# Optimization experiments

Measured on AMD Instinct MI355X. Metric: run time of the kernel, lower is better.

The kernel has to match this reference:

```python
import jax, jax.numpy as jnp
import numpy as np

B, I, H = 64, 1024, 1024
WSCALE = 0.02  # approx Xavier std for 1024-dim fan-in/out


def setup_inputs() -> dict:
    key = jax.random.key(0)
    ks = jax.random.split(key, 9)
    return {
        "input": jax.random.normal(ks[0], (B, I), jnp.float32),
        "h": jax.random.normal(ks[1], (B, H), jnp.float32),
        "C": jax.random.normal(ks[2], (B, H, H), jnp.float32),
        "weight_ih": jax.random.normal(ks[3], (3 * H, I), jnp.float32) * WSCALE,
        "weight_hh": jax.random.normal(ks[4], (3 * H, H), jnp.float32) * WSCALE,
        "bias": jnp.zeros((3 * H,), jnp.float32),
        "Wq_w": jax.random.normal(ks[5], (H, I), jnp.float32) * WSCALE,
        "Wq_b": jnp.zeros((H,), jnp.float32),
        "Wk_w": jax.random.normal(ks[6], (H, I), jnp.float32) * WSCALE,
        "Wk_b": jnp.zeros((H,), jnp.float32),
        "Wv_w": jax.random.normal(ks[7], (H, I), jnp.float32) * WSCALE,
        "Wv_b": jnp.zeros((H,), jnp.float32),
    }


def reference(input, h, C, weight_ih, weight_hh, bias, Wq_w, Wq_b, Wk_w, Wk_b, Wv_w, Wv_b):
    # gates: [B, 3H]
    gates = input @ weight_ih.T + bias + h @ weight_hh.T
    i, f, o = jnp.split(gates, 3, axis=1)
    i = jnp.exp(i)
    f = jnp.exp(f)
    o = jax.nn.sigmoid(o)
    q = input @ Wq_w.T + Wq_b
    k = input @ Wk_w.T + Wk_b
    v = input @ Wv_w.T + Wv_b
    # matrix memory update: outer product v k^T gated by i, decay by f (broadcast over columns)
    C_new = f[:, :, None] * C + i[:, :, None] * (v[:, :, None] * k[:, None, :])
    # readout: h = o * (q^T C_new), contracting q over the row (v) axis of C
    h_new = o * jnp.einsum("bi,bij->bj", q, C_new)
    return (h_new, C_new)
```

## Files before the change

### kernel.cpp

```cpp
#include <hip/hip_runtime.h>
#include <math.h>

typedef float v4 __attribute__((ext_vector_type(4)));
typedef float f32x4 __attribute__((ext_vector_type(4)));
typedef __bf16 bf16x8 __attribute__((ext_vector_type(8)));

#define HD 1024
#define NB 64

#define WS_IGT  0
#define WS_FGT  65536
#define WS_QT   131072
#define WS_VT   196608
#define WS_OGN  262144
#define WS_KN   327680
#define WS_BPK  393216
#define WS_PART 458752

__global__ __launch_bounds__(256) void k_prepb(const float* __restrict__ input,
                                               const float* __restrict__ h,
                                               float* __restrict__ ws) {
    int o = blockIdx.x * 256 + threadIdx.x;
    int l  = o & 63;
    int bt = (o >> 6) & 3;
    int ks = o >> 8;
    const float* srcm = (ks < 32) ? input : h;
    const float* src = srcm + (size_t)(bt * 16 + (l & 15)) * HD + (ks & 31) * 32 + (l >> 4) * 8;
    v4 f0 = *(const v4*)src;
    v4 f1 = *(const v4*)(src + 4);
    bf16x8 pk;
    pk[0] = (__bf16)f0.x; pk[1] = (__bf16)f0.y; pk[2] = (__bf16)f0.z; pk[3] = (__bf16)f0.w;
    pk[4] = (__bf16)f1.x; pk[5] = (__bf16)f1.y; pk[6] = (__bf16)f1.z; pk[7] = (__bf16)f1.w;
    *((bf16x8*)((__bf16*)(ws + WS_BPK)) + o) = pk;
}

__global__ __launch_bounds__(256) void k_gemm(
    const float* __restrict__ Wih, const float* __restrict__ Whh, const float* __restrict__ bias,
    const float* __restrict__ Wq, const float* __restrict__ Wqb,
    const float* __restrict__ Wk, const float* __restrict__ Wkb,
    const float* __restrict__ Wv, const float* __restrict__ Wvb,
    float* __restrict__ ws) {
    int tid  = threadIdx.x;
    int lane = tid & 63;
    int w    = tid >> 6;
    int t    = blockIdx.x;

    const bf16x8* Bp = (const bf16x8*)((const __bf16*)(ws + WS_BPK));
    __shared__ f32x4 red[4][4][64];

    f32x4 a0 = {0.f, 0.f, 0.f, 0.f};
    f32x4 a1 = a0, a2 = a0, a3 = a0;

    if (t < 192) {
        int row = t * 16 + (lane & 15);
        const float* Wb = (w < 2) ? Wih : Whh;
        const float* wrow = Wb + (size_t)row * HD + (lane >> 4) * 8;
        int cofs = (w < 2) ? 0 : -1024;
        int s0 = w * 16;
        #pragma unroll 4
        for (int s = 0; s < 16; ++s) {
            int ks = s0 + s;
            const float* ap = wrow + ks * 32 + cofs;
            v4 f0 = *(const v4*)ap;
            v4 f1 = *(const v4*)(ap + 4);
            bf16x8 a;
            a[0] = (__bf16)f0.x; a[1] = (__bf16)f0.y; a[2] = (__bf16)f0.z; a[3] = (__bf16)f0.w;
            a[4] = (__bf16)f1.x; a[5] = (__bf16)f1.y; a[6] = (__bf16)f1.z; a[7] = (__bf16)f1.w;
            const bf16x8* bb = Bp + (size_t)ks * 256 + lane;
            bf16x8 b0 = bb[0], b1 = bb[64], b2 = bb[128], b3 = bb[192];
            a0 = __builtin_amdgcn_mfma_f32_16x16x32_bf16(a, b0, a0, 0, 0, 0);
            a1 = __builtin_amdgcn_mfma_f32_16x16x32_bf16(a, b1, a1, 0, 0, 0);
            a2 = __builtin_amdgcn_mfma_f32_16x16x32_bf16(a, b2, a2, 0, 0, 0);
            a3 = __builtin_amdgcn_mfma_f32_16x16x32_bf16(a, b3, a3, 0, 0, 0);
        }
    } else {
        int t2  = t - 192;
        int sel = t2 >> 6;
        const float* W = (sel == 0) ? Wq : (sel == 1) ? Wk : Wv;
        int row = (t2 & 63) * 16 + (lane & 15);
        const float* wrow = W + (size_t)row * HD + (lane >> 4) * 8;
        int s0 = w * 8;
        #pragma unroll 4
        for (int s = 0; s < 8; ++s) {
            int ks = s0 + s;
            const float* ap = wrow + ks * 32;
            v4 f0 = *(const v4*)ap;
            v4 f1 = *(const v4*)(ap + 4);
            bf16x8 a;
            a[0] = (__bf16)f0.x; a[1] = (__bf16)f0.y; a[2] = (__bf16)f0.z; a[3] = (__bf16)f0.w;
            a[4] = (__bf16)f1.x; a[5] = (__bf16)f1.y; a[6] = (__bf16)f1.z; a[7] = (__bf16)f1.w;
            const bf16x8* bb = Bp + (size_t)ks * 256 + lane;
            bf16x8 b0 = bb[0], b1 = bb[64], b2 = bb[128], b3 = bb[192];
            a0 = __builtin_amdgcn_mfma_f32_16x16x32_bf16(a, b0, a0, 0, 0, 0);
            a1 = __builtin_amdgcn_mfma_f32_16x16x32_bf16(a, b1, a1, 0, 0, 0);
            a2 = __builtin_amdgcn_mfma_f32_16x16x32_bf16(a, b2, a2, 0, 0, 0);
            a3 = __builtin_amdgcn_mfma_f32_16x16x32_bf16(a, b3, a3, 0, 0, 0);
        }
    }

    red[w][0][lane] = a0;
    red[w][1][lane] = a1;
    red[w][2][lane] = a2;
    red[w][3][lane] = a3;
    __syncthreads();

    int b    = tid & 63;
    int rgrp = tid >> 6;
    int lane2 = (rgrp << 4) | (b & 15);
    int bt    = b >> 4;
    f32x4 s4 = red[0][bt][lane2];
    s4 += red[1][bt][lane2];
    s4 += red[2][bt][lane2];
    s4 += red[3][bt][lane2];

    if (t < 192) {
        int seg  = t >> 6;
        int rloc = (t & 63) * 16 + rgrp * 4;
        int rg   = t * 16 + rgrp * 4;
        if (seg == 0) {
            #pragma unroll
            for (int q = 0; q < 4; ++q)
                ws[WS_IGT + (rloc + q) * 64 + b] = expf(s4[q] + bias[rg + q]);
        } else if (seg == 1) {
            #pragma unroll
            for (int q = 0; q < 4; ++q)
                ws[WS_FGT + (rloc + q) * 64 + b] = expf(s4[q] + bias[rg + q]);
        } else {
            v4 o;
            #pragma unroll
            for (int q = 0; q < 4; ++q) {
                float x = s4[q] + bias[rg + q];
                o[q] = 1.f / (1.f + expf(-x));
            }
            *(v4*)(ws + WS_OGN + b * HD + rloc) = o;
        }
    } else {
        int t2   = t - 192;
        int sel  = t2 >> 6;
        int rloc = (t2 & 63) * 16 + rgrp * 4;
        const float* Bv = (sel == 0) ? Wqb : (sel == 1) ? Wkb : Wvb;
        if (sel == 0) {
            #pragma unroll
            for (int q = 0; q < 4; ++q)
                ws[WS_QT + (rloc + q) * 64 + b] = s4[q] + Bv[rloc + q];
        } else if (sel == 1) {
            v4 kv;
            #pragma unroll
            for (int q = 0; q < 4; ++q) kv[q] = s4[q] + Bv[rloc + q];
            *(v4*)(ws + WS_KN + b * HD + rloc) = kv;
        } else {
            #pragma unroll
            for (int q = 0; q < 4; ++q)
                ws[WS_VT + (rloc + q) * 64 + b] = s4[q] + Bv[rloc + q];
        }
    }
}

__global__ __launch_bounds__(256) void k_update(const float* __restrict__ C,
                                                float* __restrict__ out,
                                                float* __restrict__ ws) {
    int b  = blockIdx.x >> 5;
    int c  = blockIdx.x & 31;
    int i0 = c << 5;
    int tid = threadIdx.x;

    __shared__ float fg_s[32], iv_s[32], q_s[32];
    if (tid < 32) {
        int i = i0 + tid;
        fg_s[tid] = ws[WS_FGT + i * 64 + b];
        iv_s[tid] = ws[WS_IGT + i * 64 + b] * ws[WS_VT + i * 64 + b];
        q_s[tid]  = ws[WS_QT + i * 64 + b];
    }
    __syncthreads();

    v4 k4 = *(const v4*)(ws + WS_KN + b * HD + tid * 4);
    const v4* Cb = (const v4*)(C + (size_t)b * HD * HD) + tid;
    v4*       On = (v4*)(out + NB * HD + (size_t)b * HD * HD) + tid;
    v4 acc0 = {0.f, 0.f, 0.f, 0.f};
    v4 acc1 = {0.f, 0.f, 0.f, 0.f};

    #pragma unroll
    for (int ii = 0; ii < 32; ii += 4) {
        size_t r0 = (size_t)(i0 + ii) * 256;
        v4 c0 = __builtin_nontemporal_load(&Cb[r0]);
        v4 c1 = __builtin_nontemporal_load(&Cb[r0 + 256]);
        v4 c2 = __builtin_nontemporal_load(&Cb[r0 + 512]);
        v4 c3 = __builtin_nontemporal_load(&Cb[r0 + 768]);

        float f0 = fg_s[ii + 0], g0 = iv_s[ii + 0], q0 = q_s[ii + 0];
        float f1 = fg_s[ii + 1], g1 = iv_s[ii + 1], q1 = q_s[ii + 1];
        float f2 = fg_s[ii + 2], g2 = iv_s[ii + 2], q2 = q_s[ii + 2];
        float f3 = fg_s[ii + 3], g3 = iv_s[ii + 3], q3 = q_s[ii + 3];

        v4 n0, n1, n2, n3;
        n0.x = f0 * c0.x + g0 * k4.x; n0.y = f0 * c0.y + g0 * k4.y;
        n0.z = f0 * c0.z + g0 * k4.z; n0.w = f0 * c0.w + g0 * k4.w;
        n1.x = f1 * c1.x + g1 * k4.x; n1.y = f1 * c1.y + g1 * k4.y;
        n1.z = f1 * c1.z + g1 * k4.z; n1.w = f1 * c1.w + g1 * k4.w;
        n2.x = f2 * c2.x + g2 * k4.x; n2.y = f2 * c2.y + g2 * k4.y;
        n2.z = f2 * c2.z + g2 * k4.z; n2.w = f2 * c2.w + g2 * k4.w;
        n3.x = f3 * c3.x + g3 * k4.x; n3.y = f3 * c3.y + g3 * k4.y;
        n3.z = f3 * c3.z + g3 * k4.z; n3.w = f3 * c3.w + g3 * k4.w;

        __builtin_nontemporal_store(n0, &On[r0]);
        __builtin_nontemporal_store(n1, &On[r0 + 256]);
        __builtin_nontemporal_store(n2, &On[r0 + 512]);
        __builtin_nontemporal_store(n3, &On[r0 + 768]);

        acc0.x += q0 * n0.x; acc0.y += q0 * n0.y; acc0.z += q0 * n0.z; acc0.w += q0 * n0.w;
        acc1.x += q1 * n1.x; acc1.y += q1 * n1.y; acc1.z += q1 * n1.z; acc1.w += q1 * n1.w;
        acc0.x += q2 * n2.x; acc0.y += q2 * n2.y; acc0.z += q2 * n2.z; acc0.w += q2 * n2.w;
        acc1.x += q3 * n3.x; acc1.y += q3 * n3.y; acc1.z += q3 * n3.z; acc1.w += q3 * n3.w;
    }
    v4 acc;
    acc.x = acc0.x + acc1.x; acc.y = acc0.y + acc1.y;
    acc.z = acc0.z + acc1.z; acc.w = acc0.w + acc1.w;
    *(v4*)(ws + WS_PART + (size_t)(c * 64 + b) * HD + tid * 4) = acc;
}

__global__ __launch_bounds__(256) void k_final(float* __restrict__ out,
                                               const float* __restrict__ ws) {
    int b = blockIdx.x;
    int tid = threadIdx.x;
    const v4* part = (const v4*)(ws + WS_PART);
    v4 s = {0.f, 0.f, 0.f, 0.f};
    #pragma unroll 4
    for (int c = 0; c < 32; ++c) {
        v4 p = part[(size_t)(c * 64 + b) * 256 + tid];
        s.x += p.x; s.y += p.y; s.z += p.z; s.w += p.w;
    }
    v4 o4 = *(const v4*)(ws + WS_OGN + b * HD + tid * 4);
    v4 r;
    r.x = o4.x * s.x; r.y = o4.y * s.y; r.z = o4.z * s.z; r.w = o4.w * s.w;
    *(v4*)(out + b * HD + tid * 4) = r;
}

extern "C" void kernel_launch(void* const* d_in, const int* in_sizes, int n_in,
                              void* d_out, int out_size, void* d_ws, size_t ws_size,
                              hipStream_t stream) {
    const float* input = (const float*)d_in[0];
    const float* h     = (const float*)d_in[1];
    const float* C     = (const float*)d_in[2];
    const float* Wih   = (const float*)d_in[3];
    const float* Whh   = (const float*)d_in[4];
    const float* bias  = (const float*)d_in[5];
    const float* Wq_w  = (const float*)d_in[6];
    const float* Wq_b  = (const float*)d_in[7];
    const float* Wk_w  = (const float*)d_in[8];
    const float* Wk_b  = (const float*)d_in[9];
    const float* Wv_w  = (const float*)d_in[10];
    const float* Wv_b  = (const float*)d_in[11];
    float* out = (float*)d_out;
    float* ws  = (float*)d_ws;

    k_prepb<<<64, 256, 0, stream>>>(input, h, ws);
    k_gemm<<<384, 256, 0, stream>>>(Wih, Whh, bias, Wq_w, Wq_b, Wk_w, Wk_b, Wv_w, Wv_b, ws);
    k_update<<<2048, 256, 0, stream>>>(C, out, ws);
    k_final<<<64, 256, 0, stream>>>(out, ws);
}
```

Baseline: 480.8 us.

## Split projection GEMM into split-K waves with separate activation reduction kernel

```diff
diff --git a/kernel.cpp b/kernel.cpp
--- a/kernel.cpp
+++ b/kernel.cpp
@@ -16,6 +16,8 @@
 #define WS_KN   327680
 #define WS_BPK  393216
 #define WS_PART 458752
+#define WS_PG   2555904
+#define WS_PQ   5701632
 
 __global__ __launch_bounds__(256) void k_prepb(const float* __restrict__ input,
                                                const float* __restrict__ h,
@@ -34,125 +36,88 @@
     *((bf16x8*)((__bf16*)(ws + WS_BPK)) + o) = pk;
 }
 
-__global__ __launch_bounds__(256) void k_gemm(
-    const float* __restrict__ Wih, const float* __restrict__ Whh, const float* __restrict__ bias,
-    const float* __restrict__ Wq, const float* __restrict__ Wqb,
-    const float* __restrict__ Wk, const float* __restrict__ Wkb,
-    const float* __restrict__ Wv, const float* __restrict__ Wvb,
+__global__ __launch_bounds__(256) void k_mfma(
+    const float* __restrict__ Wih, const float* __restrict__ Whh,
+    const float* __restrict__ Wq, const float* __restrict__ Wk, const float* __restrict__ Wv,
     float* __restrict__ ws) {
-    int tid  = threadIdx.x;
-    int lane = tid & 63;
-    int w    = tid >> 6;
-    int t    = blockIdx.x;
-
+    int lane = threadIdx.x & 63;
+    int w = blockIdx.x * 4 + (threadIdx.x >> 6);
     const bf16x8* Bp = (const bf16x8*)((const __bf16*)(ws + WS_BPK));
-    __shared__ f32x4 red[4][4][64];
+
+    const float* wrow;
+    float* pout;
+    int ksB;
+    if (w < 3072) {
+        int t = w >> 4, c = w & 15;
+        const float* Wb = (c < 8) ? Wih : Whh;
+        int kk0 = (c & 7) * 128;
+        wrow = Wb + (size_t)(t * 16 + (lane & 15)) * HD + kk0 + (lane >> 4) * 8;
+        pout = ws + WS_PG + (size_t)(c * 192 + t) * 1024;
+        ksB  = c * 4;
+    } else {
+        int w2 = w - 3072;
+        int t = w2 >> 3, c = w2 & 7;
+        int sel = t >> 6;
+        const float* W = (sel == 0) ? Wq : (sel == 1) ? Wk : Wv;
+        wrow = W + (size_t)((t & 63) * 16 + (lane & 15)) * HD + c * 128 + (lane >> 4) * 8;
+        pout = ws + WS_PQ + (size_t)(c * 192 + t) * 1024;
+        ksB  = c * 4;
+    }
 
     f32x4 a0 = {0.f, 0.f, 0.f, 0.f};
     f32x4 a1 = a0, a2 = a0, a3 = a0;
-
-    if (t < 192) {
-        int row = t * 16 + (lane & 15);
-        const float* Wb = (w < 2) ? Wih : Whh;
-        const float* wrow = Wb + (size_t)row * HD + (lane >> 4) * 8;
-        int cofs = (w < 2) ? 0 : -1024;
-        int s0 = w * 16;
-        #pragma unroll 4
-        for (int s = 0; s < 16; ++s) {
-            int ks = s0 + s;
-            const float* ap = wrow + ks * 32 + cofs;
-            v4 f0 = *(const v4*)ap;
-            v4 f1 = *(const v4*)(ap + 4);
-            bf16x8 a;
-            a[0] = (__bf16)f0.x; a[1] = (__bf16)f0.y; a[2] = (__bf16)f0.z; a[3] = (__bf16)f0.w;
-            a[4] = (__bf16)f1.x; a[5] = (__bf16)f1.y; a[6] = (__bf16)f1.z; a[7] = (__bf16)f1.w;
-            const bf16x8* bb = Bp + (size_t)ks * 256 + lane;
-            bf16x8 b0 = bb[0], b1 = bb[64], b2 = bb[128], b3 = bb[192];
-            a0 = __builtin_amdgcn_mfma_f32_16x16x32_bf16(a, b0, a0, 0, 0, 0);
-            a1 = __builtin_amdgcn_mfma_f32_16x16x32_bf16(a, b1, a1, 0, 0, 0);
-            a2 = __builtin_amdgcn_mfma_f32_16x16x32_bf16(a, b2, a2, 0, 0, 0);
-            a3 = __builtin_amdgcn_mfma_f32_16x16x32_bf16(a, b3, a3, 0, 0, 0);
-        }
+    #pragma unroll
+    for (int s = 0; s < 4; ++s) {
+        const float* ap = wrow + s * 32;
+        v4 f0 = *(const v4*)ap;
+        v4 f1 = *(const v4*)(ap + 4);
+        bf16x8 a;
+        a[0] = (__bf16)f0.x; a[1] = (__bf16)f0.y; a[2] = (__bf16)f0.z; a[3] = (__bf16)f0.w;
+        a[4] = (__bf16)f1.x; a[5] = (__bf16)f1.y; a[6] = (__bf16)f1.z; a[7] = (__bf16)f1.w;
+        const bf16x8* bb = Bp + (size_t)(ksB + s) * 256 + lane;
+        bf16x8 b0 = bb[0], b1 = bb[64], b2 = bb[128], b3 = bb[192];
+        a0 = __builtin_amdgcn_mfma_f32_16x16x32_bf16(a, b0, a0, 0, 0, 0);
+        a1 = __builtin_amdgcn_mfma_f32_16x16x32_bf16(a, b1, a1, 0, 0, 0);
+        a2 = __builtin_amdgcn_mfma_f32_16x16x32_bf16(a, b2, a2, 0, 0, 0);
+        a3 = __builtin_amdgcn_mfma_f32_16x16x32_bf16(a, b3, a3, 0, 0, 0);
+    }
+    int rb = (lane >> 4) * 4, cb = lane & 15;
+    #pragma unroll
+    for (int q = 0; q < 4; ++q) {
+        pout[(rb + q) * 64 +  0 + cb] = a0[q];
+        pout[(rb + q) * 64 + 16 + cb] = a1[q];
+        pout[(rb + q) * 64 + 32 + cb] = a2[q];
+        pout[(rb + q) * 64 + 48 + cb] = a3[q];
+    }
+}
+
+__global__ __launch_bounds__(256) void k_act(
+    const float* __restrict__ bias,
+    const float* __restrict__ Wqb, const float* __restrict__ Wkb, const float* __restrict__ Wvb,
+    float* __restrict__ ws) {
+    int g = blockIdx.x * 256 + threadIdx.x;
+    if (g < 196608) {
+        int r = g >> 6, b = g & 63;
+        int t = r >> 4, ro = r & 15;
+        const float* P = ws + WS_PG + ro * 64 + b;
+        float s = bias[r];
+        #pragma unroll
+        for (int c = 0; c < 16; ++c) s += P[(size_t)(c * 192 + t) * 1024];
+        if (r < 1024)       ws[WS_IGT + r * 64 + b] = expf(s);
+        else if (r < 2048)  ws[WS_FGT + (r - 1024) * 64 + b] = expf(s);
+        else                ws[WS_OGN + b * HD + (r - 2048)] = 1.f / (1.f + expf(-s));
     } else {
-        int t2  = t - 192;
-        int sel = t2 >> 6;
-        const float* W = (sel == 0) ? Wq : (sel == 1) ? Wk : Wv;
-        int row = (t2 & 63) * 16 + (lane & 15);
-        const float* wrow = W + (size_t)row * HD + (lane >> 4) * 8;
-        int s0 = w * 8;
-        #pragma unroll 4
-        for (int s = 0; s < 8; ++s) {
-            int ks = s0 + s;
-            const float* ap = wrow + ks * 32;
-            v4 f0 = *(const v4*)ap;
-            v4 f1 = *(const v4*)(ap + 4);
-            bf16x8 a;
-            a[0] = (__bf16)f0.x; a[1] = (__bf16)f0.y; a[2] = (__bf16)f0.z; a[3] = (__bf16)f0.w;
-            a[4] = (__bf16)f1.x; a[5] = (__bf16)f1.y; a[6] = (__bf16)f1.z; a[7] = (__bf16)f1.w;
-            const bf16x8* bb = Bp + (size_t)ks * 256 + lane;
-            bf16x8 b0 = bb[0], b1 = bb[64], b2 = bb[128], b3 = bb[192];
-            a0 = __builtin_amdgcn_mfma_f32_16x16x32_bf16(a, b0, a0, 0, 0, 0);
-            a1 = __builtin_amdgcn_mfma_f32_16x16x32_bf16(a, b1, a1, 0, 0, 0);
-            a2 = __builtin_amdgcn_mfma_f32_16x16x32_bf16(a, b2, a2, 0, 0, 0);
-            a3 = __builtin_amdgcn_mfma_f32_16x16x32_bf16(a, b3, a3, 0, 0, 0);
-        }
-    }
-
-    red[w][0][lane] = a0;
-    red[w][1][lane] = a1;
-    red[w][2][lane] = a2;
-    red[w][3][lane] = a3;
-    __syncthreads();
-
-    int b    = tid & 63;
-    int rgrp = tid >> 6;
-    int lane2 = (rgrp << 4) | (b & 15);
-    int bt    = b >> 4;
-    f32x4 s4 = red[0][bt][lane2];
-    s4 += red[1][bt][lane2];
-    s4 += red[2][bt][lane2];
-    s4 += red[3][bt][lane2];
-
-    if (t < 192) {
-        int seg  = t >> 6;
-        int rloc = (t & 63) * 16 + rgrp * 4;
-        int rg   = t * 16 + rgrp * 4;
-        if (seg == 0) {
-            #pragma unroll
-            for (int q = 0; q < 4; ++q)
-                ws[WS_IGT + (rloc + q) * 64 + b] = expf(s4[q] + bias[rg + q]);
-        } else if (seg == 1) {
-            #pragma unroll
-            for (int q = 0; q < 4; ++q)
-                ws[WS_FGT + (rloc + q) * 64 + b] = expf(s4[q] + bias[rg + q]);
-        } else {
-            v4 o;
-            #pragma unroll
-            for (int q = 0; q < 4; ++q) {
-                float x = s4[q] + bias[rg + q];
-                o[q] = 1.f / (1.f + expf(-x));
-            }
-            *(v4*)(ws + WS_OGN + b * HD + rloc) = o;
-        }
-    } else {
-        int t2   = t - 192;
-        int sel  = t2 >> 6;
-        int rloc = (t2 & 63) * 16 + rgrp * 4;
-        const float* Bv = (sel == 0) ? Wqb : (sel == 1) ? Wkb : Wvb;
-        if (sel == 0) {
-            #pragma unroll
-            for (int q = 0; q < 4; ++q)
-                ws[WS_QT + (rloc + q) * 64 + b] = s4[q] + Bv[rloc + q];
-        } else if (sel == 1) {
-            v4 kv;
-            #pragma unroll
-            for (int q = 0; q < 4; ++q) kv[q] = s4[q] + Bv[rloc + q];
-            *(v4*)(ws + WS_KN + b * HD + rloc) = kv;
-        } else {
-            #pragma unroll
-            for (int q = 0; q < 4; ++q)
-                ws[WS_VT + (rloc + q) * 64 + b] = s4[q] + Bv[rloc + q];
-        }
+        int e = g - 196608;
+        int r2 = e >> 6, b = e & 63;
+        int t = r2 >> 4, ro = r2 & 15;
+        int sel = r2 >> 10, rr = r2 & 1023;
+        const float* P = ws + WS_PQ + ro * 64 + b;
+        float s = ((sel == 0) ? Wqb : (sel == 1) ? Wkb : Wvb)[rr];
+        #pragma unroll
+        for (int c = 0; c < 8; ++c) s += P[(size_t)(c * 192 + t) * 1024];
+        if (sel == 0)      ws[WS_QT + rr * 64 + b] = s;
+        else if (sel == 1) ws[WS_KN + b * HD + rr] = s;
+        else               ws[WS_VT + rr * 64 + b] = s;
     }
 }
 
@@ -254,7 +219,8 @@
     float* ws  = (float*)d_ws;
 
     k_prepb<<<64, 256, 0, stream>>>(input, h, ws);
-    k_gemm<<<384, 256, 0, stream>>>(Wih, Whh, bias, Wq_w, Wq_b, Wk_w, Wk_b, Wv_w, Wv_b, ws);
+    k_mfma<<<1152, 256, 0, stream>>>(Wih, Whh, Wq_w, Wk_w, Wv_w, ws);
+    k_act<<<1536, 256, 0, stream>>>(bias, Wq_b, Wk_b, Wv_b, ws);
     k_update<<<2048, 256, 0, stream>>>(C, out, ws);
     k_final<<<64, 256, 0, stream>>>(out, ws);
 }
```

Result: no change. 488.2 us (+1.6%).

## Software-pipeline C loads in update kernel and drop nontemporal hints

Applied to the files above, without the earlier changes.

```diff
diff --git a/kernel.cpp b/kernel.cpp
--- a/kernel.cpp
+++ b/kernel.cpp
@@ -174,43 +174,44 @@
     __syncthreads();
 
     v4 k4 = *(const v4*)(ws + WS_KN + b * HD + tid * 4);
-    const v4* Cb = (const v4*)(C + (size_t)b * HD * HD) + tid;
-    v4*       On = (v4*)(out + NB * HD + (size_t)b * HD * HD) + tid;
+    const v4* Cb = (const v4*)(C + (size_t)b * HD * HD) + (size_t)i0 * 256 + tid;
+    v4*       On = (v4*)(out + NB * HD + (size_t)b * HD * HD) + (size_t)i0 * 256 + tid;
     v4 acc0 = {0.f, 0.f, 0.f, 0.f};
     v4 acc1 = {0.f, 0.f, 0.f, 0.f};
 
-    #pragma unroll
+    v4 c0 = Cb[0], c1 = Cb[256], c2 = Cb[512], c3 = Cb[768];
+    #pragma unroll 1
     for (int ii = 0; ii < 32; ii += 4) {
-        size_t r0 = (size_t)(i0 + ii) * 256;
-        v4 c0 = __builtin_nontemporal_load(&Cb[r0]);
-        v4 c1 = __builtin_nontemporal_load(&Cb[r0 + 256]);
-        v4 c2 = __builtin_nontemporal_load(&Cb[r0 + 512]);
-        v4 c3 = __builtin_nontemporal_load(&Cb[r0 + 768]);
-
-        float f0 = fg_s[ii + 0], g0 = iv_s[ii + 0], q0 = q_s[ii + 0];
-        float f1 = fg_s[ii + 1], g1 = iv_s[ii + 1], q1 = q_s[ii + 1];
-        float f2 = fg_s[ii + 2], g2 = iv_s[ii + 2], q2 = q_s[ii + 2];
-        float f3 = fg_s[ii + 3], g3 = iv_s[ii + 3], q3 = q_s[ii + 3];
-
-        v4 n0, n1, n2, n3;
-        n0.x = f0 * c0.x + g0 * k4.x; n0.y = f0 * c0.y + g0 * k4.y;
-        n0.z = f0 * c0.z + g0 * k4.z; n0.w = f0 * c0.w + g0 * k4.w;
-        n1.x = f1 * c1.x + g1 * k4.x; n1.y = f1 * c1.y + g1 * k4.y;
-        n1.z = f1 * c1.z + g1 * k4.z; n1.w = f1 * c1.w + g1 * k4.w;
-        n2.x = f2 * c2.x + g2 * k4.x; n2.y = f2 * c2.y + g2 * k4.y;
-        n2.z = f2 * c2.z + g2 * k4.z; n2.w = f2 * c2.w + g2 * k4.w;
-        n3.x = f3 * c3.x + g3 * k4.x; n3.y = f3 * c3.y + g3 * k4.y;
-        n3.z = f3 * c3.z + g3 * k4.z; n3.w = f3 * c3.w + g3 * k4.w;
-
-        __builtin_nontemporal_store(n0, &On[r0]);
-        __builtin_nontemporal_store(n1, &On[r0 + 256]);
-        __builtin_nontemporal_store(n2, &On[r0 + 512]);
-        __builtin_nontemporal_store(n3, &On[r0 + 768]);
-
-        acc0.x += q0 * n0.x; acc0.y += q0 * n0.y; acc0.z += q0 * n0.z; acc0.w += q0 * n0.w;
-        acc1.x += q1 * n1.x; acc1.y += q1 * n1.y; acc1.z += q1 * n1.z; acc1.w += q1 * n1.w;
-        acc0.x += q2 * n2.x; acc0.y += q2 * n2.y; acc0.z += q2 * n2.z; acc0.w += q2 * n2.w;
-        acc1.x += q3 * n3.x; acc1.y += q3 * n3.y; acc1.z += q3 * n3.z; acc1.w += q3 * n3.w;
+        v4 p0, p1, p2, p3;
+        if (ii < 28) {
+            size_t rn = (size_t)(ii + 4) * 256;
+            p0 = Cb[rn]; p1 = Cb[rn + 256]; p2 = Cb[rn + 512]; p3 = Cb[rn + 768];
+        }
+        v4 fv = *(const v4*)&fg_s[ii];
+        v4 gv = *(const v4*)&iv_s[ii];
+        v4 qv = *(const v4*)&q_s[ii];
+
+        c0.x = fv.x * c0.x + gv.x * k4.x; c0.y = fv.x * c0.y + gv.x * k4.y;
+        c0.z = fv.x * c0.z + gv.x * k4.z; c0.w = fv.x * c0.w + gv.x * k4.w;
+        c1.x = fv.y * c1.x + gv.y * k4.x; c1.y = fv.y * c1.y + gv.y * k4.y;
+        c1.z = fv.y * c1.z + gv.y * k4.z; c1.w = fv.y * c1.w + gv.y * k4.w;
+        c2.x = fv.z * c2.x + gv.z * k4.x; c2.y = fv.z * c2.y + gv.z * k4.y;
+        c2.z = fv.z * c2.z + gv.z * k4.z; c2.w = fv.z * c2.w + gv.z * k4.w;
+        c3.x = fv.w * c3.x + gv.w * k4.x; c3.y = fv.w * c3.y + gv.w * k4.y;
+        c3.z = fv.w * c3.z + gv.w * k4.z; c3.w = fv.w * c3.w + gv.w * k4.w;
+
+        size_t r0 = (size_t)ii * 256;
+        On[r0]       = c0;
+        On[r0 + 256] = c1;
+        On[r0 + 512] = c2;
+        On[r0 + 768] = c3;
+
+        acc0.x += qv.x * c0.x; acc0.y += qv.x * c0.y; acc0.z += qv.x * c0.z; acc0.w += qv.x * c0.w;
+        acc1.x += qv.y * c1.x; acc1.y += qv.y * c1.y; acc1.z += qv.y * c1.z; acc1.w += qv.y * c1.w;
+        acc0.x += qv.z * c2.x; acc0.y += qv.z * c2.y; acc0.z += qv.z * c2.z; acc0.w += qv.z * c2.w;
+        acc1.x += qv.w * c3.x; acc1.y += qv.w * c3.y; acc1.z += qv.w * c3.z; acc1.w += qv.w * c3.w;
+
+        c0 = p0; c1 = p1; c2 = p2; c3 = p3;
     }
     v4 acc;
     acc.x = acc0.x + acc1.x; acc.y = acc0.y + acc1.y;
```

Result: slower. 502.8 us (+4.6%).
